# Kernel optimization log

Hardware: AMD Instinct MI355X
Metric: run time of the kernel (lower is better)

Reference implementation:

```python
import jax, jax.numpy as jnp
import numpy as np

NEG_SLOPE = 0.01  # torch F.leaky_relu default

def _leaky(x):
    return jnp.where(x >= 0, x, NEG_SLOPE * x)

def _gcn(x, W, b, src, dst, w, n):
    # GCNConv(add_self_loops=False, normalize=False):
    # h = x @ W; out[dst] += w * h[src]; out += b
    h = x @ W
    agg = jax.ops.segment_sum(w[:, None] * h[src], dst, num_segments=n)
    return agg + b

def setup_inputs() -> dict:
    key = jax.random.key(0)
    ks = jax.random.split(key, 10)
    N, E, IN, HID, OUT, B = 100000, 300000, 256, 256, 256, 128
    features = jax.random.normal(ks[0], (N, IN), dtype=jnp.float32)
    values = jax.random.uniform(ks[1], (E,), dtype=jnp.float32)
    s = 1.0 / np.sqrt(IN)
    W1 = jax.random.normal(ks[2], (IN, HID), dtype=jnp.float32) * s
    b1 = jnp.zeros((HID,), dtype=jnp.float32)
    W2 = jax.random.normal(ks[3], (HID + IN, OUT), dtype=jnp.float32) * (1.0 / np.sqrt(HID + IN))
    b2 = jnp.zeros((OUT,), dtype=jnp.float32)
    Wl = jax.random.normal(ks[4], (HID + OUT, IN), dtype=jnp.float32) * (1.0 / np.sqrt(HID + OUT))
    bl = jnp.zeros((IN,), dtype=jnp.float32)
    adjs = jax.random.randint(ks[5], (2, E), 0, N, dtype=jnp.int64)
    batch = jnp.sort(jax.random.randint(ks[6], (N,), 0, B, dtype=jnp.int64))
    root_idx = jax.random.randint(ks[7], (B,), 0, N, dtype=jnp.int64)
    return {"features": features, "values": values, "W1": W1, "b1": b1,
            "W2": W2, "b2": b2, "Wl": Wl, "bl": bl,
            "adjs": adjs, "batch": batch, "root_idx": root_idx}

def reference(features, values, W1, b1, W2, b2, Wl, bl, adjs, batch, root_idx):
    N = features.shape[0]
    src, dst = adjs[0], adjs[1]
    f1 = features  # [N, in]
    h = _gcn(f1, W1, b1, src, dst, values, N)  # conv1 -> [N, hid]
    f2 = h
    # root_extend: per-batch broadcast of root features == gather f1[root_idx[batch]]
    root1 = f1[root_idx[batch]]  # [N, in]
    x = _leaky(jnp.concatenate([h, root1], axis=1))
    # dropout is identity at inference
    x = _gcn(x, W2, b2, src, dst, values, N)  # conv2 -> [N, out]
    x = _leaky(x)
    root2 = f2[root_idx[batch]]  # [N, hid]
    x = jnp.concatenate([x, root2], axis=1)
    return _leaky(x @ Wl + bl)  # [N, in]
```

## Files before the change

kernel.cpp:

```cpp
#include <hip/hip_runtime.h>

typedef short short8 __attribute__((ext_vector_type(8)));
typedef float floatx4 __attribute__((ext_vector_type(4)));

#define LEAKY(v) ((v) >= 0.0f ? (v) : 0.01f * (v))

constexpr int D = 256;

__device__ __forceinline__ short f2bf(float x) {
  unsigned u = __float_as_uint(x);
  u += 0x7fffu + ((u >> 16) & 1u);
  return (short)(u >> 16);
}
__device__ __forceinline__ float bf2f(short s) {
  return __uint_as_float(((unsigned)(unsigned short)s) << 16);
}

#define AS1 __attribute__((address_space(1)))
#define AS3 __attribute__((address_space(3)))

__device__ __forceinline__ void gload_lds16(const void* g, void* lds) {
  __builtin_amdgcn_global_load_lds((const AS1 void*)g, (AS3 void*)lds, 16, 0, 0);
}

__global__ void transpose_w(const float* __restrict__ W1,
                            const float* __restrict__ W2,
                            const float* __restrict__ Wl,
                            short* __restrict__ Wt) {
  __shared__ float t[32][33];
  const float* src = (blockIdx.z == 0) ? W1 : (blockIdx.z == 1) ? W2 : Wl;
  short* dst = Wt + (size_t)blockIdx.z * D * D;
  int tx = threadIdx.x, ty = threadIdx.y;
  t[ty][tx] = src[(size_t)(blockIdx.y * 32 + ty) * D + blockIdx.x * 32 + tx];
  __syncthreads();
  dst[(size_t)(blockIdx.x * 32 + ty) * D + blockIdx.y * 32 + tx] =
      f2bf(t[tx][ty]);
}

__global__ __launch_bounds__(256) void conv_bf(const float* __restrict__ X,
                                               short* __restrict__ Y,
                                               long n8) {
  long i = (long)blockIdx.x * 256 + threadIdx.x;
  const long stride = (long)gridDim.x * 256;
  for (; i < n8; i += stride) {
    float4 v0 = ((const float4*)X)[2 * i];
    float4 v1 = ((const float4*)X)[2 * i + 1];
    short8 s;
    s[0] = f2bf(v0.x); s[1] = f2bf(v0.y); s[2] = f2bf(v0.z); s[3] = f2bf(v0.w);
    s[4] = f2bf(v1.x); s[5] = f2bf(v1.y); s[6] = f2bf(v1.z); s[7] = f2bf(v1.w);
    ((short8*)Y)[i] = s;
  }
}

template <bool ADD_ROW, bool FINAL>
__global__ __launch_bounds__(512, 2) void gemm_pipe(
    const short* __restrict__ A, const short* __restrict__ Wt,
    const float* __restrict__ R, const int* __restrict__ batch,
    const float* __restrict__ bias, void* __restrict__ Cvoid, int M,
    int nTiles) {
  __shared__ __align__(16) short As[2][64 * 256];
  const int tid = threadIdx.x;
  const int l = tid & 63, w = tid >> 6, lm = l & 15, q = l >> 4;
  const int ncol0 = w * 32;

  short8 bf[2][8];
#pragma unroll
  for (int j = 0; j < 2; j++)
#pragma unroll
    for (int kk = 0; kk < 8; kk++)
      bf[j][kk] = *(const short8*)(Wt + (size_t)(ncol0 + j * 16 + lm) * D +
                                   kk * 32 + q * 8);
#pragma unroll
  for (int j = 0; j < 2; j++)
#pragma unroll
    for (int kk = 0; kk < 8; kk++)
      asm volatile("" : "+v"(bf[j][kk]));

  float4 b4[2];
  if (FINAL) {
#pragma unroll
    for (int j = 0; j < 2; j++)
      b4[j] = *(const float4*)(bias + ncol0 + j * 16 + q * 4);
  }

  const int stride = gridDim.x;
  int t = blockIdx.x;
  int p = 0;

  auto stage = [&](int tile, int buf) {
#pragma unroll
    for (int r = 0; r < 4; r++) {
      const int s = r * 8 + w;
      const int kk = s >> 2, i = s & 3;
      int grow = tile * 64 + i * 16 + lm;
      grow = grow < M ? grow : M - 1;
      const char* src = (const char*)A + (size_t)grow * 512 + kk * 64 + q * 16;
      gload_lds16(src, (char*)(&As[buf][0]) + s * 1024);
    }
  };

  if (t < nTiles) stage(t, 0);

  for (; t < nTiles; t += stride) {
    __syncthreads();
    const int nxt = t + stride;
    if (nxt < nTiles) stage(nxt, p ^ 1);

    floatx4 acc[4][2];
#pragma unroll
    for (int i = 0; i < 4; i++)
#pragma unroll
      for (int j = 0; j < 2; j++) acc[i][j] = (floatx4){0.f, 0.f, 0.f, 0.f};

    const char* base = (const char*)(&As[p][0]) + (size_t)l * 16;
#pragma unroll
    for (int kk = 0; kk < 8; kk++) {
      short8 a[4];
#pragma unroll
      for (int i = 0; i < 4; i++)
        a[i] = *(const short8*)(base + (kk * 4 + i) * 1024);
#pragma unroll
      for (int i = 0; i < 4; i++)
#pragma unroll
        for (int j = 0; j < 2; j++)
          acc[i][j] = __builtin_amdgcn_mfma_f32_16x16x32_bf16(
              bf[j][kk], a[i], acc[i][j], 0, 0, 0);
    }

    const int rowBase = t * 64;
#pragma unroll
    for (int i = 0; i < 4; i++) {
      const int row = rowBase + i * 16 + lm;
      if (row < M) {
        int rb = 0;
        if (ADD_ROW) rb = batch[row];
#pragma unroll
        for (int j = 0; j < 2; j++) {
          const int col0 = ncol0 + j * 16 + q * 4;
          float c0 = acc[i][j][0], c1 = acc[i][j][1], c2 = acc[i][j][2],
                c3 = acc[i][j][3];
          if (ADD_ROW) {
            float4 rv = *(const float4*)(R + (size_t)rb * D + col0);
            c0 += rv.x; c1 += rv.y; c2 += rv.z; c3 += rv.w;
          }
          if (!FINAL) {
            uint2 o;
            o.x = (unsigned)(unsigned short)f2bf(c0) |
                  ((unsigned)(unsigned short)f2bf(c1) << 16);
            o.y = (unsigned)(unsigned short)f2bf(c2) |
                  ((unsigned)(unsigned short)f2bf(c3) << 16);
            *(uint2*)((short*)Cvoid + (size_t)row * D + col0) = o;
          } else {
            c0 += b4[j].x; c1 += b4[j].y; c2 += b4[j].z; c3 += b4[j].w;
            c0 = LEAKY(c0); c1 = LEAKY(c1); c2 = LEAKY(c2); c3 = LEAKY(c3);
            float4 o = {c0, c1, c2, c3};
            *(float4*)((float*)Cvoid + (size_t)row * D + col0) = o;
          }
        }
      }
    }
    p ^= 1;
  }
}

__global__ void count_dst(const int* __restrict__ dst, int* __restrict__ offs,
                          int E) {
  int e = blockIdx.x * 256 + threadIdx.x;
  if (e < E) atomicAdd(&offs[dst[e]], 1);
}

__global__ void scan_blocks(int* __restrict__ offs, int* __restrict__ bsums,
                            int n) {
  __shared__ int tmp[256];
  int i = blockIdx.x * 256 + threadIdx.x;
  int v = (i < n) ? offs[i] : 0;
  tmp[threadIdx.x] = v;
  __syncthreads();
  for (int off = 1; off < 256; off <<= 1) {
    int t = (threadIdx.x >= off) ? tmp[threadIdx.x - off] : 0;
    __syncthreads();
    tmp[threadIdx.x] += t;
    __syncthreads();
  }
  if (i < n) offs[i] = tmp[threadIdx.x] - v;
  if (threadIdx.x == 255) bsums[blockIdx.x] = tmp[255];
}

__global__ void scan_sums(int* __restrict__ bs, int nb) {
  __shared__ int tmp[1024];
  int v = (threadIdx.x < nb) ? bs[threadIdx.x] : 0;
  tmp[threadIdx.x] = v;
  __syncthreads();
  for (int off = 1; off < 1024; off <<= 1) {
    int t = (threadIdx.x >= off) ? tmp[threadIdx.x - off] : 0;
    __syncthreads();
    tmp[threadIdx.x] += t;
    __syncthreads();
  }
  if (threadIdx.x < nb) bs[threadIdx.x] = tmp[threadIdx.x] - v;
}

__global__ void add_offsets(int* __restrict__ offs, const int* __restrict__ bs,
                            int n, int* __restrict__ cursor) {
  int i = blockIdx.x * 256 + threadIdx.x;
  if (i < n) {
    int o = offs[i] + bs[blockIdx.x];
    offs[i] = o;
    cursor[i] = o;
  }
}

__global__ void fill_buckets(const int* __restrict__ src,
                             const int* __restrict__ dst,
                             const float* __restrict__ vals,
                             int* __restrict__ cursor, int* __restrict__ esrc,
                             float* __restrict__ ew, int E) {
  int e = blockIdx.x * 256 + threadIdx.x;
  if (e < E) {
    int p = atomicAdd(&cursor[dst[e]], 1);
    esrc[p] = src[e];
    ew[p] = vals[e];
  }
}

__global__ __launch_bounds__(256) void aggregate_bf(
    const short* __restrict__ H, const int* __restrict__ offs,
    const int* __restrict__ esrc, const float* __restrict__ ew,
    const float* __restrict__ bias, short* __restrict__ out, int N, int E) {
  int node = blockIdx.x * 4 + (threadIdx.x >> 6);
  if (node >= N) return;
  int lane = threadIdx.x & 63;
  int beg = offs[node];
  int end = (node == N - 1) ? E : offs[node + 1];
  float a0 = 0.f, a1 = 0.f, a2 = 0.f, a3 = 0.f;
  for (int i = beg; i < end; i++) {
    int s = esrc[i];
    float wv = ew[i];
    uint2 pk = ((const uint2*)(H + (size_t)s * D))[lane];
    a0 += wv * bf2f((short)(pk.x & 0xffff));
    a1 += wv * bf2f((short)(pk.x >> 16));
    a2 += wv * bf2f((short)(pk.y & 0xffff));
    a3 += wv * bf2f((short)(pk.y >> 16));
  }
  float4 b = ((const float4*)bias)[lane];
  a0 = LEAKY(a0 + b.x);
  a1 = LEAKY(a1 + b.y);
  a2 = LEAKY(a2 + b.z);
  a3 = LEAKY(a3 + b.w);
  uint2 o;
  o.x = (unsigned)(unsigned short)f2bf(a0) |
        ((unsigned)(unsigned short)f2bf(a1) << 16);
  o.y = (unsigned)(unsigned short)f2bf(a2) |
        ((unsigned)(unsigned short)f2bf(a3) << 16);
  ((uint2*)(out + (size_t)node * D))[lane] = o;
}

__global__ void root_gemm1(const float* __restrict__ X,
                           const int* __restrict__ root_idx,
                           const float* __restrict__ W2,
                           float* __restrict__ R1) {
  __shared__ float a[D];
  int b = blockIdx.x, j = threadIdx.x;
  int r = root_idx[b];
  a[j] = LEAKY(X[(size_t)r * D + j]);
  __syncthreads();
  float acc = 0.f;
#pragma unroll 8
  for (int k = 0; k < D; k++) acc += a[k] * W2[(size_t)(D + k) * D + j];
  R1[b * D + j] = acc;
}

__global__ void root_gemm2(const short* __restrict__ H,
                           const int* __restrict__ root_idx,
                           const int* __restrict__ offs,
                           const int* __restrict__ esrc,
                           const float* __restrict__ ew,
                           const float* __restrict__ b1,
                           const float* __restrict__ Wl, float* __restrict__ R2,
                           int N, int E) {
  __shared__ float a[D];
  int b = blockIdx.x, j = threadIdx.x;
  int r = root_idx[b];
  int beg = offs[r], end = (r == N - 1) ? E : offs[r + 1];
  float acc = b1[j];
  for (int e = beg; e < end; e++)
    acc += ew[e] * bf2f(H[(size_t)esrc[e] * D + j]);
  a[j] = acc;
  __syncthreads();
  float s = 0.f;
#pragma unroll 8
  for (int k = 0; k < D; k++) s += a[k] * Wl[(size_t)(D + k) * D + j];
  R2[b * D + j] = s;
}

extern "C" void kernel_launch(void* const* d_in, const int* in_sizes, int n_in,
                              void* d_out, int out_size, void* d_ws,
                              size_t ws_size, hipStream_t stream) {
  const float* features = (const float*)d_in[0];
  const float* values   = (const float*)d_in[1];
  const float* W1 = (const float*)d_in[2];
  const float* b1 = (const float*)d_in[3];
  const float* W2 = (const float*)d_in[4];
  const float* b2 = (const float*)d_in[5];
  const float* Wl = (const float*)d_in[6];
  const float* bl = (const float*)d_in[7];
  const int* adjs = (const int*)d_in[8];
  const int* batch = (const int*)d_in[9];
  const int* root_idx = (const int*)d_in[10];

  const int N = in_sizes[0] / D;
  const int E = in_sizes[1];
  const int B = in_sizes[10];
  const int* srcI = adjs;
  const int* dstI = adjs + E;

  short* bf0 = (short*)d_ws;
  short* bf1 = bf0 + (size_t)N * D;
  short* Wt = bf1 + (size_t)N * D;
  float* R1 = (float*)(Wt + (size_t)3 * D * D);
  float* R2 = R1 + (size_t)B * D;
  float* ew = R2 + (size_t)B * D;
  int* offs = (int*)(ew + E);
  int* cursor = offs + N;
  int* esrc = cursor + N;
  int* bsums = esrc + E;

  const int nb = (N + 255) / 256;

  hipMemsetAsync(offs, 0, (size_t)N * sizeof(int), stream);
  count_dst<<<(E + 255) / 256, 256, 0, stream>>>(dstI, offs, E);
  scan_blocks<<<nb, 256, 0, stream>>>(offs, bsums, N);
  scan_sums<<<1, 1024, 0, stream>>>(bsums, nb);
  add_offsets<<<nb, 256, 0, stream>>>(offs, bsums, N, cursor);
  fill_buckets<<<(E + 255) / 256, 256, 0, stream>>>(srcI, dstI, values, cursor,
                                                    esrc, ew, E);

  transpose_w<<<dim3(8, 8, 3), dim3(32, 32), 0, stream>>>(W1, W2, Wl, Wt);

  conv_bf<<<2048, 256, 0, stream>>>(features, bf1, (long)N * D / 8);

  const int nTiles = (N + 63) / 64;
  const int ggrid = 256;
  const int aggGrid = (N + 3) / 4;

  gemm_pipe<false, false><<<ggrid, 512, 0, stream>>>(
      bf1, Wt, nullptr, nullptr, nullptr, bf0, N, nTiles);

  aggregate_bf<<<aggGrid, 256, 0, stream>>>(bf0, offs, esrc, ew, b1, bf1, N, E);

  root_gemm1<<<B, 256, 0, stream>>>(features, root_idx, W2, R1);
  root_gemm2<<<B, 256, 0, stream>>>(bf0, root_idx, offs, esrc, ew, b1, Wl, R2,
                                    N, E);

  gemm_pipe<true, false><<<ggrid, 512, 0, stream>>>(
      bf1, Wt + (size_t)D * D, R1, batch, nullptr, bf0, N, nTiles);

  aggregate_bf<<<aggGrid, 256, 0, stream>>>(bf0, offs, esrc, ew, b2, bf1, N, E);

  gemm_pipe<true, true><<<ggrid, 512, 0, stream>>>(
      bf1, Wt + (size_t)2 * D * D, R2, batch, bl, (float*)d_out, N, nTiles);
}
```

Baseline: 479.8 us.

## Halve GEMM row tile, unroll edge aggregation, merge root GEMM kernels

```diff
diff --git a/kernel.cpp b/kernel.cpp
--- a/kernel.cpp
+++ b/kernel.cpp
@@ -58,7 +58,7 @@
     const float* __restrict__ R, const int* __restrict__ batch,
     const float* __restrict__ bias, void* __restrict__ Cvoid, int M,
     int nTiles) {
-  __shared__ __align__(16) short As[2][64 * 256];
+  __shared__ __align__(16) short As[2][32 * 256];
   const int tid = threadIdx.x;
   const int l = tid & 63, w = tid >> 6, lm = l & 15, q = l >> 4;
   const int ncol0 = w * 32;
@@ -89,10 +89,10 @@
 
   auto stage = [&](int tile, int buf) {
 #pragma unroll
-    for (int r = 0; r < 4; r++) {
+    for (int r = 0; r < 2; r++) {
       const int s = r * 8 + w;
-      const int kk = s >> 2, i = s & 3;
-      int grow = tile * 64 + i * 16 + lm;
+      const int kk = s >> 1, i = s & 1;
+      int grow = tile * 32 + i * 16 + lm;
       grow = grow < M ? grow : M - 1;
       const char* src = (const char*)A + (size_t)grow * 512 + kk * 64 + q * 16;
       gload_lds16(src, (char*)(&As[buf][0]) + s * 1024);
@@ -106,30 +106,30 @@
     const int nxt = t + stride;
     if (nxt < nTiles) stage(nxt, p ^ 1);
 
-    floatx4 acc[4][2];
-#pragma unroll
-    for (int i = 0; i < 4; i++)
+    floatx4 acc[2][2];
+#pragma unroll
+    for (int i = 0; i < 2; i++)
 #pragma unroll
       for (int j = 0; j < 2; j++) acc[i][j] = (floatx4){0.f, 0.f, 0.f, 0.f};
 
     const char* base = (const char*)(&As[p][0]) + (size_t)l * 16;
 #pragma unroll
     for (int kk = 0; kk < 8; kk++) {
-      short8 a[4];
-#pragma unroll
-      for (int i = 0; i < 4; i++)
-        a[i] = *(const short8*)(base + (kk * 4 + i) * 1024);
-#pragma unroll
-      for (int i = 0; i < 4; i++)
+      short8 a[2];
+#pragma unroll
+      for (int i = 0; i < 2; i++)
+        a[i] = *(const short8*)(base + (kk * 2 + i) * 1024);
+#pragma unroll
+      for (int i = 0; i < 2; i++)
 #pragma unroll
         for (int j = 0; j < 2; j++)
           acc[i][j] = __builtin_amdgcn_mfma_f32_16x16x32_bf16(
               bf[j][kk], a[i], acc[i][j], 0, 0, 0);
     }
 
-    const int rowBase = t * 64;
-#pragma unroll
-    for (int i = 0; i < 4; i++) {
+    const int rowBase = t * 32;
+#pragma unroll
+    for (int i = 0; i < 2; i++) {
       const int row = rowBase + i * 16 + lm;
       if (row < M) {
         int rb = 0;
@@ -233,7 +233,18 @@
   int beg = offs[node];
   int end = (node == N - 1) ? E : offs[node + 1];
   float a0 = 0.f, a1 = 0.f, a2 = 0.f, a3 = 0.f;
-  for (int i = beg; i < end; i++) {
+  int i = beg;
+  for (; i + 1 < end; i += 2) {
+    int s0 = esrc[i], s1 = esrc[i + 1];
+    float w0 = ew[i], w1 = ew[i + 1];
+    uint2 p0 = ((const uint2*)(H + (size_t)s0 * D))[lane];
+    uint2 p1 = ((const uint2*)(H + (size_t)s1 * D))[lane];
+    a0 += w0 * bf2f((short)(p0.x & 0xffff)) + w1 * bf2f((short)(p1.x & 0xffff));
+    a1 += w0 * bf2f((short)(p0.x >> 16))    + w1 * bf2f((short)(p1.x >> 16));
+    a2 += w0 * bf2f((short)(p0.y & 0xffff)) + w1 * bf2f((short)(p1.y & 0xffff));
+    a3 += w0 * bf2f((short)(p0.y >> 16))    + w1 * bf2f((short)(p1.y >> 16));
+  }
+  if (i < end) {
     int s = esrc[i];
     float wv = ew[i];
     uint2 pk = ((const uint2*)(H + (size_t)s * D))[lane];
@@ -255,42 +266,41 @@
   ((uint2*)(out + (size_t)node * D))[lane] = o;
 }
 
-__global__ void root_gemm1(const float* __restrict__ X,
-                           const int* __restrict__ root_idx,
-                           const float* __restrict__ W2,
-                           float* __restrict__ R1) {
+__global__ void root_both(const float* __restrict__ X,
+                          const int* __restrict__ root_idx,
+                          const float* __restrict__ W2, float* __restrict__ R1,
+                          const short* __restrict__ H,
+                          const int* __restrict__ offs,
+                          const int* __restrict__ esrc,
+                          const float* __restrict__ ew,
+                          const float* __restrict__ b1,
+                          const float* __restrict__ Wl, float* __restrict__ R2,
+                          int N, int E, int B) {
   __shared__ float a[D];
-  int b = blockIdx.x, j = threadIdx.x;
-  int r = root_idx[b];
-  a[j] = LEAKY(X[(size_t)r * D + j]);
-  __syncthreads();
-  float acc = 0.f;
+  int j = threadIdx.x;
+  if ((int)blockIdx.x < B) {
+    int b = blockIdx.x;
+    int r = root_idx[b];
+    a[j] = LEAKY(X[(size_t)r * D + j]);
+    __syncthreads();
+    float acc = 0.f;
 #pragma unroll 8
-  for (int k = 0; k < D; k++) acc += a[k] * W2[(size_t)(D + k) * D + j];
-  R1[b * D + j] = acc;
-}
-
-__global__ void root_gemm2(const short* __restrict__ H,
-                           const int* __restrict__ root_idx,
-                           const int* __restrict__ offs,
-                           const int* __restrict__ esrc,
-                           const float* __restrict__ ew,
-                           const float* __restrict__ b1,
-                           const float* __restrict__ Wl, float* __restrict__ R2,
-                           int N, int E) {
-  __shared__ float a[D];
-  int b = blockIdx.x, j = threadIdx.x;
-  int r = root_idx[b];
-  int beg = offs[r], end = (r == N - 1) ? E : offs[r + 1];
-  float acc = b1[j];
-  for (int e = beg; e < end; e++)
-    acc += ew[e] * bf2f(H[(size_t)esrc[e] * D + j]);
-  a[j] = acc;
-  __syncthreads();
-  float s = 0.f;
+    for (int k = 0; k < D; k++) acc += a[k] * W2[(size_t)(D + k) * D + j];
+    R1[b * D + j] = acc;
+  } else {
+    int b = blockIdx.x - B;
+    int r = root_idx[b];
+    int beg = offs[r], end = (r == N - 1) ? E : offs[r + 1];
+    float acc = b1[j];
+    for (int e = beg; e < end; e++)
+      acc += ew[e] * bf2f(H[(size_t)esrc[e] * D + j]);
+    a[j] = acc;
+    __syncthreads();
+    float s = 0.f;
 #pragma unroll 8
-  for (int k = 0; k < D; k++) s += a[k] * Wl[(size_t)(D + k) * D + j];
-  R2[b * D + j] = s;
+    for (int k = 0; k < D; k++) s += a[k] * Wl[(size_t)(D + k) * D + j];
+    R2[b * D + j] = s;
+  }
 }
 
 extern "C" void kernel_launch(void* const* d_in, const int* in_sizes, int n_in,
@@ -339,8 +349,8 @@
 
   conv_bf<<<2048, 256, 0, stream>>>(features, bf1, (long)N * D / 8);
 
-  const int nTiles = (N + 63) / 64;
-  const int ggrid = 256;
+  const int nTiles = (N + 31) / 32;
+  const int ggrid = 512;
   const int aggGrid = (N + 3) / 4;
 
   gemm_pipe<false, false><<<ggrid, 512, 0, stream>>>(
@@ -348,9 +358,8 @@
 
   aggregate_bf<<<aggGrid, 256, 0, stream>>>(bf0, offs, esrc, ew, b1, bf1, N, E);
 
-  root_gemm1<<<B, 256, 0, stream>>>(features, root_idx, W2, R1);
-  root_gemm2<<<B, 256, 0, stream>>>(bf0, root_idx, offs, esrc, ew, b1, Wl, R2,
-                                    N, E);
+  root_both<<<2 * B, 256, 0, stream>>>(features, root_idx, W2, R1, bf0, offs,
+                                       esrc, ew, b1, Wl, R2, N, E, B);
 
   gemm_pipe<true, false><<<ggrid, 512, 0, stream>>>(
       bf1, Wt + (size_t)D * D, R1, batch, nullptr, bf0, N, nTiles);
```

Result: faster. 434.2 us (-9.5%).
